# Optimization experiments

Measured on AMD Instinct MI355X. Metric: run time of the kernel, lower is better.

Reference implementation:

```python
import jax, jax.numpy as jnp
import numpy as np

N, Q, E, D = 100000, 128, 500000, 32
D4 = 4 * D
RATIO_UPDATE = 0.2
NEG_SLOPE = 0.01  # LeakyReLU default


def setup_inputs() -> dict:
    key = jax.random.key(0)
    ks = jax.random.split(key, 16)
    return {
        "visited_node_score": jax.random.uniform(ks[0], (N,), jnp.float32),
        "node_repr": jax.random.normal(ks[1], (N, D), jnp.float32),
        "eg0": jnp.sort(jax.random.randint(ks[2], (E,), 0, Q)),
        "src0": jax.random.randint(ks[3], (E,), 0, N),
        "dst0": jax.random.randint(ks[4], (E,), 0, N),
        "rel0": jax.random.normal(ks[5], (E, D), jnp.float32),
        "eg1": jnp.sort(jax.random.randint(ks[6], (E,), 0, Q)),
        "src1": jax.random.randint(ks[7], (E,), 0, N),
        "dst1": jax.random.randint(ks[8], (E,), 0, N),
        "rel1": jax.random.normal(ks[9], (E, D), jnp.float32),
        "query_src_emb": jax.random.normal(ks[10], (Q, D), jnp.float32),
        "query_rel_emb": jax.random.normal(ks[11], (Q, D), jnp.float32),
        "Wq": jax.random.normal(ks[12], (D4, D4), jnp.float32) * np.sqrt(2.0 / D4).astype(np.float32),
        "Wk": jax.random.normal(ks[13], (D4, D4), jnp.float32) * np.sqrt(2.0 / D4).astype(np.float32),
        "Wlin": jax.random.normal(ks[14], (D, D), jnp.float32) * np.sqrt(2.0 / (2 * D)).astype(np.float32),
        "blin": jnp.zeros((D,), jnp.float32),
        "max_edges": 500,
    }


def segment_softmax(logits, seg, num_segments):
    # softmax within groups of identical seg id (source node index)
    m = jax.ops.segment_max(logits, seg, num_segments=num_segments)
    ex = jnp.exp(logits - m[seg])
    s = jax.ops.segment_sum(ex, seg, num_segments=num_segments)
    return ex / s[seg]


def segment_topk_mask(values, seg, k):
    # keep mask for per-segment top-k (seg must be sorted); stable -> first occurrence on ties
    n = values.shape[0]
    order = jnp.lexsort((-values, seg))  # primary: seg, secondary: descending value
    seg_sorted = seg[order]
    idx = jnp.arange(n)
    is_start = jnp.concatenate([jnp.array([True]), seg_sorted[1:] != seg_sorted[:-1]])
    seg_start = jax.lax.cummax(jnp.where(is_start, idx, 0))
    rank_sorted = idx - seg_start  # rank within segment, 0 = largest
    rank = jnp.zeros((n,), jnp.int32).at[order].set(rank_sorted.astype(jnp.int32))
    return rank < k


def reference(visited_node_score, node_repr, eg0, src0, dst0, rel0,
              eg1, src1, dst1, rel1, query_src_emb, query_rel_emb,
              Wq, Wk, Wlin, blin, max_edges):
    def att_logits(repr_, src, dst, eg, rel):
        q = query_src_emb[eg]
        r = query_rel_emb[eg]
        left = jnp.concatenate([repr_[src], rel, q, r], axis=-1)   # [E, 4D]
        right = jnp.concatenate([repr_[dst], rel, q, r], axis=-1)  # [E, 4D]
        return jnp.sum((left @ Wq.T) * (right @ Wk.T), axis=-1)    # [E]

    num_nodes = node_repr.shape[0]

    # ---- last layer: attention + segmented top-k pruning ----
    logits1 = att_logits(node_repr, src1, dst1, eg1, rel1)
    w1 = segment_softmax(logits1, src1, num_nodes)           # softmax over out-edges of each src node
    src_score = visited_node_score[src1]
    target_score = w1 * src_score
    keep = segment_topk_mask(target_score, eg1, max_edges)   # top-k per eg_idx
    w1p = jnp.where(keep, w1, 0.0)

    # node score aggregation == 'sum': score[n] = sum_{kept e: dst=n} w * src_score
    updated_node_score = jax.ops.segment_sum(w1p * src_score, dst1, num_segments=num_nodes)

    # representation update along pruned edges (linear_act=False)
    agg = jax.ops.segment_sum(w1p[:, None] * node_repr[src1], dst1, num_segments=num_nodes)
    repr_ = (1.0 - RATIO_UPDATE) * agg + RATIO_UPDATE * node_repr

    # ---- earlier layer(s), no pruning ----
    logits0 = att_logits(repr_, src0, dst0, eg0, rel0)
    w0 = segment_softmax(logits0, src0, num_nodes)
    agg0 = jax.ops.segment_sum(w0[:, None] * repr_[src0], dst0, num_segments=num_nodes)
    repr_ = (1.0 - RATIO_UPDATE) * agg0 + RATIO_UPDATE * repr_

    # bypass_forward: LeakyReLU(Linear(repr))
    h = repr_ @ Wlin.T + blin
    updated_repr = jnp.where(h >= 0, h, NEG_SLOPE * h)
    return updated_node_score, updated_repr
```

## Files before the change

### kernel.cpp

```cpp
#include <hip/hip_runtime.h>
#include <math.h>

#define DD 32
#define DD4 128
#define TPB 256
#define LDSCAP 6144
#define CANDCAP 2048

__device__ __forceinline__ unsigned long long dsort_key(double x) {
  unsigned long long b = (unsigned long long)__double_as_longlong(x);
  return (b & 0x8000000000000000ull) ? ~b : (b | 0x8000000000000000ull);
}
__device__ __forceinline__ double dunsort_key(unsigned long long k) {
  unsigned long long b = (k & 0x8000000000000000ull) ? (k ^ 0x8000000000000000ull) : ~k;
  return __longlong_as_double((long long)b);
}
__device__ __forceinline__ unsigned int fsort_key(float x) {
  unsigned int b = __float_as_uint(x);
  return (b & 0x80000000u) ? ~b : (b | 0x80000000u);
}
__device__ __forceinline__ float funsort_key(unsigned int k) {
  unsigned int b = (k & 0x80000000u) ? (k ^ 0x80000000u) : ~k;
  return __uint_as_float(b);
}

__device__ __forceinline__ int block_iscan256(int x, int* wsum) {
  const int lane = threadIdx.x & 63, w = threadIdx.x >> 6;
#pragma unroll
  for (int o = 1; o < 64; o <<= 1) {
    int y = __shfl_up(x, o, 64);
    if (lane >= o) x += y;
  }
  if (lane == 63) wsum[w] = x;
  __syncthreads();
  int add = 0;
#pragma unroll
  for (int i = 0; i < 4; ++i) add += (i < w) ? wsum[i] : 0;
  __syncthreads();
  return x + add;
}

__global__ __launch_bounds__(TPB) void k_precompute_M(
    const float* __restrict__ Wq, const float* __restrict__ Wk,
    double* __restrict__ M64) {
  int t = blockIdx.x * blockDim.x + threadIdx.x;
  int i = t >> 7, j = t & 127;
  double acc = 0.0;
  for (int k = 0; k < DD4; ++k)
    acc += (double)Wq[k * DD4 + i] * (double)Wk[k * DD4 + j];
  M64[i * DD4 + j] = acc;
}

__global__ __launch_bounds__(TPB) void k_sym22(
    const double* __restrict__ M64, double* __restrict__ S64) {
  int i = blockIdx.x * blockDim.x + threadIdx.x;
  int r = i >> 5, c = i & 31;
  double g  = M64[(32 + r) * DD4 + 32 + c];
  double gt = M64[(32 + c) * DD4 + 32 + r];
  S64[i] = (c > r) ? (g + gt) : ((c == r) ? g : 0.0);
}

__global__ __launch_bounds__(64) void k_per_query(
    const double* __restrict__ M64,
    const float* __restrict__ qemb, const float* __restrict__ remb,
    double* __restrict__ p64, double* __restrict__ pD64, double* __restrict__ c64,
    float* __restrict__ p32, float* __restrict__ pD32, float* __restrict__ c32) {
  int q = blockIdx.x;
  int l = threadIdx.x;
  __shared__ double qr[64];
  qr[l] = (l < DD) ? (double)qemb[q * DD + l] : (double)remb[q * DD + (l - DD)];
  __syncthreads();
  double a = 0.0;
  for (int j = 0; j < 64; ++j) a += M64[l * DD4 + 64 + j] * qr[j];
  double ct = 0.0;
  for (int j = 0; j < 64; ++j) ct += M64[(64 + j) * DD4 + l] * qr[j];
  if (l >= DD) a += ct;
  p64[q * 64 + l] = a;
  p32[q * 64 + l] = (float)a;
  if (l < DD) {
    pD64[q * DD + l] = ct;
    pD32[q * DD + l] = (float)ct;
  }
  double a3 = 0.0;
  for (int j = 0; j < 64; ++j) a3 += M64[(64 + l) * DD4 + 64 + j] * qr[j];
  a3 *= qr[l];
  for (int o = 32; o; o >>= 1) a3 += __shfl_xor(a3, o);
  if (l == 0) { c64[q] = a3; c32[q] = (float)a3; }
}

template <typename T, bool MIX>
__global__ __launch_bounds__(TPB) void k_node_pre(
    const double* __restrict__ M64, const float* __restrict__ reprIn,
    const float* __restrict__ aggIn, float* __restrict__ reprOut,
    float* __restrict__ t, float* __restrict__ u, float* __restrict__ v, int N_) {
  __shared__ T GT[3 * 32 * 32];
  for (int i = threadIdx.x; i < 1024; i += TPB) {
    int j = i >> 5, c = i & 31;
    GT[i]        = (T)M64[c * DD4 + j];
    GT[1024 + i] = (T)M64[j * DD4 + 32 + c];
    GT[2048 + i] = (T)M64[(32 + c) * DD4 + j];
  }
  __syncthreads();
  const int base = blockIdx.x * 32;
  const int sub = threadIdx.x >> 5;
  const int c = threadIdx.x & 31;
#pragma unroll
  for (int m = 0; m < 4; ++m) {
    const int n = base + m * 8 + sub;
    if (n >= N_) continue;
    float h = reprIn[(size_t)n * DD + c];
    if constexpr (MIX) {
      float a = aggIn[(size_t)n * DD + c];
      h = 0.8f * a + 0.2f * h;
      reprOut[(size_t)n * DD + c] = h;
    }
    T ta = (T)0, ua = (T)0, va = (T)0;
#pragma unroll
    for (int j = 0; j < 32; ++j) {
      T hj = (T)__shfl(h, j, 32);
      ta += GT[j * 32 + c] * hj;
      ua += GT[1024 + j * 32 + c] * hj;
      va += GT[2048 + j * 32 + c] * hj;
    }
    t[(size_t)n * DD + c] = (float)ta;
    u[(size_t)n * DD + c] = (float)ua;
    v[(size_t)n * DD + c] = (float)va;
  }
}

template <typename T>
__global__ __launch_bounds__(TPB) void k_quad(
    const double* __restrict__ S64,
    const float* __restrict__ rel, const int* __restrict__ eg,
    const T* __restrict__ pq, const T* __restrict__ cq,
    T* __restrict__ quad, int E) {
  __shared__ T Ss[32 * 32];
  for (int i = threadIdx.x; i < 1024; i += TPB) Ss[i] = (T)S64[i];
  __syncthreads();
  const int e = blockIdx.x * TPB + threadIdx.x;
  if (e >= E) return;
  const int q = eg[e];
  T rl[32];
  {
    const float4* r4 = (const float4*)rel + (size_t)e * 8;
#pragma unroll
    for (int j = 0; j < 8; ++j) {
      float4 x = r4[j];
      rl[4 * j] = (T)x.x; rl[4 * j + 1] = (T)x.y;
      rl[4 * j + 2] = (T)x.z; rl[4 * j + 3] = (T)x.w;
    }
  }
  const T* prow = pq + (size_t)q * 64 + 32;
  T lin0 = (T)0, lin1 = (T)0;
#pragma unroll
  for (int i = 0; i < 32; i += 2) {
    lin0 += prow[i] * rl[i];
    lin1 += prow[i + 1] * rl[i + 1];
  }
  T a0 = cq[q] + lin0, a1 = lin1, a2 = (T)0, a3 = (T)0;
#pragma unroll
  for (int i = 0; i < 32; ++i) {
    T r0 = Ss[i * 32 + i] * rl[i];
    T r1 = (T)0;
#pragma unroll
    for (int j = i + 1; j < 32; ++j) {
      if ((j - i) & 1) r1 += Ss[i * 32 + j] * rl[j];
      else             r0 += Ss[i * 32 + j] * rl[j];
    }
    T rr = (r0 + r1) * rl[i];
    if ((i & 3) == 0) a0 += rr;
    else if ((i & 3) == 1) a1 += rr;
    else if ((i & 3) == 2) a2 += rr;
    else a3 += rr;
  }
  quad[e] = (a0 + a1) + (a2 + a3);
}

template <typename T>
__global__ __launch_bounds__(TPB) void k_edge_dots(
    const float* __restrict__ repr, const float* __restrict__ rel,
    const int* __restrict__ src, const int* __restrict__ dst, const int* __restrict__ eg,
    const float* __restrict__ tvec, const float* __restrict__ uvec, const float* __restrict__ vvec,
    const T* __restrict__ pq, const T* __restrict__ pDq, const T* __restrict__ quad,
    T* __restrict__ logits, void* __restrict__ mkey, int E) {
  const long long t = (long long)blockIdx.x * TPB + threadIdx.x;
  const int e = (int)(t >> 3), part = (int)(t & 7);
  if (e >= E) return;
  const int s = src[e], d = dst[e], q = eg[e];
  const float4 hs = ((const float4*)repr)[(size_t)s * 8 + part];
  const float4 td = ((const float4*)tvec)[(size_t)d * 8 + part];
  const float4 hd = ((const float4*)repr)[(size_t)d * 8 + part];
  const float4 rl = ((const float4*)rel)[(size_t)e * 8 + part];
  const float4 us = ((const float4*)uvec)[(size_t)s * 8 + part];
  const float4 vd = ((const float4*)vvec)[(size_t)d * 8 + part];
  const T* p  = pq  + (size_t)q * 64 + part * 4;
  const T* pD = pDq + (size_t)q * DD + part * 4;
  T a = (T)hs.x * ((T)td.x + p[0]) + (T)hs.y * ((T)td.y + p[1]) +
        (T)hs.z * ((T)td.z + p[2]) + (T)hs.w * ((T)td.w + p[3]);
  a += (T)hd.x * pD[0] + (T)hd.y * pD[1] + (T)hd.z * pD[2] + (T)hd.w * pD[3];
  a += (T)rl.x * (T)(us.x + vd.x) + (T)rl.y * (T)(us.y + vd.y) +
       (T)rl.z * (T)(us.z + vd.z) + (T)rl.w * (T)(us.w + vd.w);
  a += __shfl_xor(a, 1);
  a += __shfl_xor(a, 2);
  a += __shfl_xor(a, 4);
  if (part == 0) {
    a += quad[e];
    logits[e] = a;
    if constexpr (sizeof(T) == 8) {
      atomicMax((unsigned long long*)mkey + s, dsort_key((double)a));
    } else {
      atomicMax((unsigned int*)mkey + s, fsort_key((float)a));
    }
  }
}

__global__ __launch_bounds__(TPB) void k_expsum64(
    double* __restrict__ io, const unsigned long long* __restrict__ mkey,
    const int* __restrict__ src, double* __restrict__ ssum, int E) {
  int e = blockIdx.x * blockDim.x + threadIdx.x;
  if (e >= E) return;
  int s = src[e];
  double ex = exp(io[e] - dunsort_key(mkey[s]));
  io[e] = ex;
  atomicAdd(&ssum[s], ex);
}
__global__ __launch_bounds__(TPB) void k_expsum32h(
    float* __restrict__ io, const unsigned int* __restrict__ mkey,
    const int* __restrict__ src, const int* __restrict__ dst,
    float* __restrict__ ssum, int* __restrict__ cnt, int E) {
  int e = blockIdx.x * blockDim.x + threadIdx.x;
  if (e >= E) return;
  int s = src[e];
  float ex = expf(io[e] - funsort_key(mkey[s]));
  io[e] = ex;
  atomicAdd(&ssum[s], ex);
  atomicAdd(&cnt[dst[e]], 1);
}

__global__ __launch_bounds__(TPB) void k_weights_target(
    const double* __restrict__ ex, const double* __restrict__ ssum,
    const int* __restrict__ src, const float* __restrict__ score,
    const int* __restrict__ eg, int* __restrict__ qoff,
    float* __restrict__ w1f, unsigned int* __restrict__ tkey, int E, int Q) {
  int e = blockIdx.x * blockDim.x + threadIdx.x;
  if (e >= E) return;
  int s = src[e];
  double w = ex[e] / ssum[s];
  float wf = (float)w;
  w1f[e] = wf;
  float tgt = wf * score[s];
  tkey[e] = fsort_key(tgt);
  int cur = eg[e];
  int prev = (e == 0) ? -1 : eg[e - 1];
  for (int v = prev + 1; v <= cur; ++v) qoff[v] = e;
  if (e == E - 1) {
    for (int v = cur + 1; v <= Q; ++v) qoff[v] = E;
  }
}

__global__ __launch_bounds__(TPB) void k_topk(
    const unsigned int* __restrict__ tkey, const float* __restrict__ w1f,
    const int* __restrict__ qoff, const int* __restrict__ maxe,
    float* __restrict__ w1p, int E) {
  __shared__ unsigned int keys[LDSCAP];
  __shared__ int hist[256];
  __shared__ unsigned short cand[CANDCAP];
  __shared__ int wsum[4];
  __shared__ int sh_cnt;
  __shared__ unsigned int sh_prefix;
  __shared__ int sh_need;
  const int q = blockIdx.x;
  const int s = qoff[q], e2 = qoff[q + 1];
  const int n = e2 - s;
  const int K = maxe[0];
  if (n <= K) {
    for (int i = s + threadIdx.x; i < e2; i += TPB) w1p[i] = w1f[i];
    return;
  }
  const bool useLds = (n <= LDSCAP);
  if (useLds) {
    for (int i = threadIdx.x; i < n; i += TPB) keys[i] = tkey[s + i];
  }
  hist[threadIdx.x] = 0;
  __syncthreads();
  for (int i = threadIdx.x; i < n; i += TPB) {
    unsigned int k = useLds ? keys[i] : tkey[s + i];
    atomicAdd(&hist[k >> 24], 1);
  }
  __syncthreads();
  int need = K;
  {
    int h = hist[255 - threadIdx.x];
    int incl = block_iscan256(h, wsum);
    int excl = incl - h;
    if (incl >= need && excl < need) {
      sh_prefix = (unsigned int)(255 - threadIdx.x) << 24;
      sh_need = need - excl;
    }
  }
  __syncthreads();
  unsigned int prefix = sh_prefix;
  need = sh_need;
  const int cnt0 = hist[prefix >> 24];
  const bool compact = useLds && (cnt0 <= CANDCAP);
  if (threadIdx.x == 0) sh_cnt = 0;
  __syncthreads();
  if (compact) {
    const unsigned int d0 = prefix >> 24;
    for (int i = threadIdx.x; i < n; i += TPB) {
      if ((keys[i] >> 24) == d0) {
        int p = atomicAdd(&sh_cnt, 1);
        cand[p] = (unsigned short)i;
      }
    }
  }
  __syncthreads();
  const int ncand = compact ? sh_cnt : 0;
  for (int pass = 1; pass < 4; ++pass) {
    const int shift = 24 - 8 * pass;
    const unsigned int himask = 0xFFFFFFFFu << (shift + 8);
    hist[threadIdx.x] = 0;
    __syncthreads();
    if (compact) {
      for (int ci = threadIdx.x; ci < ncand; ci += TPB) {
        unsigned int k = keys[cand[ci]];
        if ((k & himask) == prefix) atomicAdd(&hist[(k >> shift) & 255], 1);
      }
    } else {
      for (int i = threadIdx.x; i < n; i += TPB) {
        unsigned int k = useLds ? keys[i] : tkey[s + i];
        if ((k & himask) == prefix) atomicAdd(&hist[(k >> shift) & 255], 1);
      }
    }
    __syncthreads();
    int h = hist[255 - threadIdx.x];
    int incl = block_iscan256(h, wsum);
    int excl = incl - h;
    if (incl >= need && excl < need) {
      sh_prefix = prefix | ((unsigned int)(255 - threadIdx.x) << shift);
      sh_need = need - excl;
    }
    __syncthreads();
    prefix = sh_prefix;
    need = sh_need;
    __syncthreads();
  }
  const unsigned int kth = prefix;
  const int r = need;
  const int C = (n + TPB - 1) / TPB;
  const int b0 = min(threadIdx.x * C, n);
  const int b1 = min(b0 + C, n);
  int myt = 0;
  for (int i = b0; i < b1; ++i) {
    unsigned int k = useLds ? keys[i] : tkey[s + i];
    myt += (k == kth) ? 1 : 0;
  }
  int tincl = block_iscan256(myt, wsum);
  int tiepre = tincl - myt;
  for (int i = b0; i < b1; ++i) {
    unsigned int k = useLds ? keys[i] : tkey[s + i];
    float v = 0.f;
    if (k > kth) {
      v = w1f[s + i];
    } else if (k == kth) {
      if (tiepre < r) v = w1f[s + i];
      ++tiepre;
    }
    w1p[s + i] = v;
  }
}

__global__ __launch_bounds__(TPB) void k_apply1(
    const float* __restrict__ w1p, const int* __restrict__ src, const int* __restrict__ dst,
    const float* __restrict__ repr0, const float* __restrict__ score,
    float* __restrict__ agg, float* __restrict__ score_out, int E) {
  int t = blockIdx.x * blockDim.x + threadIdx.x;
  int e = t >> 3, part = t & 7;
  if (e >= E) return;
  float w = w1p[e];
  if (w == 0.f) return;
  int sv = src[e], dv = dst[e];
  const float4 rv = ((const float4*)repr0)[sv * 8 + part];
  float* ap = agg + (size_t)dv * DD + part * 4;
  atomicAdd(ap + 0, w * rv.x);
  atomicAdd(ap + 1, w * rv.y);
  atomicAdd(ap + 2, w * rv.z);
  atomicAdd(ap + 3, w * rv.w);
  if (part == 0) atomicAdd(score_out + dv, w * score[sv]);
}

#define SCHUNK 1024
__global__ __launch_bounds__(TPB) void k_scan1(
    const int* __restrict__ cnt, int* __restrict__ off, int* __restrict__ bsum, int N_) {
  __shared__ int sd[TPB];
  const int b = blockIdx.x, t = threadIdx.x;
  const int base = b * SCHUNK + t * 4;
  int v[4];
  int s4 = 0;
#pragma unroll
  for (int k = 0; k < 4; ++k) {
    v[k] = (base + k < N_) ? cnt[base + k] : 0;
    s4 += v[k];
  }
  sd[t] = s4;
  __syncthreads();
  for (int o = 1; o < TPB; o <<= 1) {
    int x = (t >= o) ? sd[t - o] : 0;
    __syncthreads();
    sd[t] += x;
    __syncthreads();
  }
  int excl = sd[t] - s4;
  if (t == TPB - 1) bsum[b] = sd[t];
  int run = excl;
#pragma unroll
  for (int k = 0; k < 4; ++k) {
    if (base + k < N_) { off[base + k] = run; run += v[k]; }
  }
}

__global__ __launch_bounds__(TPB) void k_scan2(
    int* __restrict__ bsum, int* __restrict__ off, int nblk, int N_, int E) {
  __shared__ int wsum[4];
  if (nblk <= TPB) {
    int t = threadIdx.x;
    int x = (t < nblk) ? bsum[t] : 0;
    int orig = x;
    const int lane = t & 63, w = t >> 6;
#pragma unroll
    for (int o = 1; o < 64; o <<= 1) {
      int y = __shfl_up(x, o, 64);
      if (lane >= o) x += y;
    }
    if (lane == 63) wsum[w] = x;
    __syncthreads();
    int add = 0;
#pragma unroll
    for (int i = 0; i < 4; ++i) add += (i < w) ? wsum[i] : 0;
    x += add;
    if (t < nblk) bsum[t] = x - orig;
    if (t == 0) off[N_] = E;
  } else {
    if (threadIdx.x != 0) return;
    int run = 0;
    for (int i = 0; i < nblk; ++i) { int tmp = bsum[i]; bsum[i] = run; run += tmp; }
    off[N_] = E;
  }
}

__global__ __launch_bounds__(TPB) void k_scan3(
    int* __restrict__ off, const int* __restrict__ bsum, int* __restrict__ cursor, int N_) {
  int i = blockIdx.x * blockDim.x + threadIdx.x;
  if (i >= N_) return;
  int v = off[i] + bsum[i >> 10];
  off[i] = v;
  cursor[i] = v;
}

__global__ __launch_bounds__(TPB) void k_scatter0(
    const float* __restrict__ ex, const float* __restrict__ ssum,
    const int* __restrict__ src, const int* __restrict__ dst,
    int* __restrict__ cursor, float2* __restrict__ pk, int E) {
  int e = blockIdx.x * blockDim.x + threadIdx.x;
  if (e >= E) return;
  int s = src[e];
  float w = ex[e] / ssum[s];
  int pos = atomicAdd(&cursor[dst[e]], 1);
  pk[pos] = make_float2(w, __int_as_float(s));
}

__global__ __launch_bounds__(TPB) void k_gather_final(
    const float2* __restrict__ pk, const int* __restrict__ off,
    const float* __restrict__ repr1,
    const float* __restrict__ Wlin, const float* __restrict__ blin,
    float* __restrict__ out_repr, int N_) {
  __shared__ float WsT[DD * DD];
  __shared__ float bs[DD];
  for (int i = threadIdx.x; i < DD * DD; i += TPB) {
    int r = i >> 5, c = i & 31;
    WsT[c * DD + r] = Wlin[i];
  }
  if (threadIdx.x < DD) bs[threadIdx.x] = blin[threadIdx.x];
  __syncthreads();
  const int n = blockIdx.x * 8 + (threadIdx.x >> 5);
  const int c = threadIdx.x & 31;
  if (n >= N_) return;
  float acc = 0.f;
  const int j1 = off[n + 1];
  for (int j = off[n]; j < j1; ++j) {
    float2 p = pk[j];
    int s = __float_as_int(p.y);
    acc += p.x * repr1[(size_t)s * DD + c];
  }
  float mix = 0.8f * acc + 0.2f * repr1[(size_t)n * DD + c];
  float o = bs[c];
#pragma unroll 8
  for (int j = 0; j < DD; ++j) {
    float mj = __shfl(mix, j, 32);
    o += WsT[j * DD + c] * mj;
  }
  out_repr[(size_t)n * DD + c] = (o >= 0.f) ? o : 0.01f * o;
}

extern "C" void kernel_launch(void* const* d_in, const int* in_sizes, int n_in,
                              void* d_out, int out_size, void* d_ws, size_t ws_size,
                              hipStream_t stream) {
  (void)n_in; (void)out_size; (void)ws_size;
  const float* score = (const float*)d_in[0];
  const float* nrepr = (const float*)d_in[1];
  const int*   eg0   = (const int*)d_in[2];
  const int*   src0  = (const int*)d_in[3];
  const int*   dst0  = (const int*)d_in[4];
  const float* rel0  = (const float*)d_in[5];
  const int*   eg1   = (const int*)d_in[6];
  const int*   src1  = (const int*)d_in[7];
  const int*   dst1  = (const int*)d_in[8];
  const float* rel1  = (const float*)d_in[9];
  const float* qemb  = (const float*)d_in[10];
  const float* remb  = (const float*)d_in[11];
  const float* Wq    = (const float*)d_in[12];
  const float* Wk    = (const float*)d_in[13];
  const float* Wlin  = (const float*)d_in[14];
  const float* blin  = (const float*)d_in[15];
  const int*   maxe  = (const int*)d_in[16];

  const int N_ = in_sizes[0];
  const int E_ = in_sizes[2];
  const int Q_ = in_sizes[10] / DD;

  char* wsc = (char*)d_ws;
  size_t off = 0;
  auto alloc = [&](size_t bytes) -> void* {
    void* p = wsc + off;
    off += (bytes + 255) & ~(size_t)255;
    return p;
  };
  double* M64  = (double*)alloc((size_t)DD4 * DD4 * 8);
  double* S64  = (double*)alloc((size_t)DD * DD * 8);
  double* p64  = (double*)alloc((size_t)Q_ * 64 * 8);
  double* pD64 = (double*)alloc((size_t)Q_ * DD * 8);
  double* c64  = (double*)alloc((size_t)Q_ * 8);
  float*  p32  = (float*)alloc((size_t)Q_ * 64 * 4);
  float*  pD32 = (float*)alloc((size_t)Q_ * DD * 4);
  float*  c32  = (float*)alloc((size_t)Q_ * 4);
  int*    qoff = (int*)alloc((size_t)(Q_ + 2) * 4);
  double* lg1  = (double*)alloc((size_t)E_ * 8);
  double* qv64 = (double*)alloc((size_t)E_ * 8);
  float*  w1f  = (float*)alloc((size_t)E_ * 4);
  unsigned int* tkey = (unsigned int*)alloc((size_t)E_ * 4);
  float*  w1p  = (float*)alloc((size_t)E_ * 4);
  float*  lg0  = (float*)alloc((size_t)E_ * 4);
  float*  repr1 = (float*)alloc((size_t)N_ * DD * 4);
  float*  tvec = (float*)alloc((size_t)N_ * DD * 4);
  float*  uvec = (float*)alloc((size_t)N_ * DD * 4);
  float*  vvec = (float*)alloc((size_t)N_ * DD * 4);
  size_t zstart = off;
  unsigned long long* mkey1 = (unsigned long long*)alloc((size_t)N_ * 8);
  double* s1   = (double*)alloc((size_t)N_ * 8);
  float*  agg  = (float*)alloc((size_t)N_ * DD * 4);
  unsigned int* mkey0 = (unsigned int*)alloc((size_t)N_ * 4);
  float*  s0   = (float*)alloc((size_t)N_ * 4);
  size_t zlen = off - zstart;

  float* qv32 = (float*)qv64;

  int* cnt    = (int*)tvec;
  int* offcsr = (int*)tvec + N_;
  int* cursor = (int*)tvec + 2 * (size_t)N_ + 64;
  int* bsum   = (int*)tvec + 3 * (size_t)N_ + 128;
  float2* pk  = (float2*)uvec;

  float* out_score = (float*)d_out;
  float* out_repr  = out_score + N_;

  hipMemsetAsync(wsc + zstart, 0, zlen, stream);
  hipMemsetAsync(d_out, 0, (size_t)N_ * 4, stream);

  k_precompute_M<<<(DD4 * DD4) / TPB, TPB, 0, stream>>>(Wq, Wk, M64);
  k_sym22<<<4, TPB, 0, stream>>>(M64, S64);
  k_per_query<<<Q_, 64, 0, stream>>>(M64, qemb, remb, p64, pD64, c64, p32, pD32, c32);

  const int ngrid = (N_ + TPB - 1) / TPB;
  const int n32grid = (N_ + 31) / 32;
  const int egrid = (E_ + TPB - 1) / TPB;
  const int dgrid = (int)(((size_t)E_ * 8 + TPB - 1) / TPB);

  k_node_pre<double, false><<<n32grid, TPB, 0, stream>>>(M64, nrepr, nullptr, nullptr,
                                                         tvec, uvec, vvec, N_);
  k_quad<double><<<egrid, TPB, 0, stream>>>(S64, rel1, eg1, p64, c64, qv64, E_);
  k_edge_dots<double><<<dgrid, TPB, 0, stream>>>(nrepr, rel1, src1, dst1, eg1,
                                                 tvec, uvec, vvec, p64, pD64, qv64,
                                                 lg1, (void*)mkey1, E_);
  k_expsum64<<<egrid, TPB, 0, stream>>>(lg1, mkey1, src1, s1, E_);
  k_weights_target<<<egrid, TPB, 0, stream>>>(lg1, s1, src1, score, eg1, qoff,
                                              w1f, tkey, E_, Q_);
  k_topk<<<Q_, TPB, 0, stream>>>(tkey, w1f, qoff, maxe, w1p, E_);

  k_apply1<<<dgrid, TPB, 0, stream>>>(w1p, src1, dst1, nrepr, score, agg, out_score, E_);

  k_node_pre<float, true><<<n32grid, TPB, 0, stream>>>(M64, nrepr, agg, repr1,
                                                       tvec, uvec, vvec, N_);
  k_quad<float><<<egrid, TPB, 0, stream>>>(S64, rel0, eg0, p32, c32, qv32, E_);
  k_edge_dots<float><<<dgrid, TPB, 0, stream>>>(repr1, rel0, src0, dst0, eg0,
                                                tvec, uvec, vvec, p32, pD32, qv32,
                                                lg0, (void*)mkey0, E_);

  hipMemsetAsync(cnt, 0, (size_t)N_ * 4, stream);
  k_expsum32h<<<egrid, TPB, 0, stream>>>(lg0, mkey0, src0, dst0, s0, cnt, E_);
  const int nblk = (N_ + SCHUNK - 1) / SCHUNK;
  k_scan1<<<nblk, TPB, 0, stream>>>(cnt, offcsr, bsum, N_);
  k_scan2<<<1, TPB, 0, stream>>>(bsum, offcsr, nblk, N_, E_);
  k_scan3<<<ngrid, TPB, 0, stream>>>(offcsr, bsum, cursor, N_);
  k_scatter0<<<egrid, TPB, 0, stream>>>(lg0, s0, src0, dst0, cursor, pk, E_);
  k_gather_final<<<(N_ + 7) / 8, TPB, 0, stream>>>(pk, offcsr, repr1, Wlin, blin, out_repr, N_);
}
```

Measured before the change: 688.5 us.

## Restructure node projection to one node per thread with uniform matrix reads

k_node_pre now assigns one node per thread. Each thread holds its 32-element representation in registers and reads the projection matrices directly from global memory with thread-uniform addresses, replacing the LDS-staged matrix and per-element warp shuffles. Outputs are transposed through LDS so global stores stay coalesced as float4. k_quad also drops its LDS staging of the symmetric matrix and reads it uniformly from global, and float32 copies of M and S are precomputed so the float passes skip per-block double-to-float conversion. This adds register pressure (32 accumulator inputs plus 8 partial sums) and several extra block barriers per kernel.

```diff
diff --git a/kernel.cpp b/kernel.cpp
--- a/kernel.cpp
+++ b/kernel.cpp
@@ -42,22 +42,25 @@
 
 __global__ __launch_bounds__(TPB) void k_precompute_M(
     const float* __restrict__ Wq, const float* __restrict__ Wk,
-    double* __restrict__ M64) {
+    double* __restrict__ M64, float* __restrict__ M32) {
   int t = blockIdx.x * blockDim.x + threadIdx.x;
   int i = t >> 7, j = t & 127;
   double acc = 0.0;
   for (int k = 0; k < DD4; ++k)
     acc += (double)Wq[k * DD4 + i] * (double)Wk[k * DD4 + j];
   M64[i * DD4 + j] = acc;
+  M32[i * DD4 + j] = (float)acc;
 }
 
 __global__ __launch_bounds__(TPB) void k_sym22(
-    const double* __restrict__ M64, double* __restrict__ S64) {
+    const double* __restrict__ M64, double* __restrict__ S64, float* __restrict__ S32) {
   int i = blockIdx.x * blockDim.x + threadIdx.x;
   int r = i >> 5, c = i & 31;
   double g  = M64[(32 + r) * DD4 + 32 + c];
   double gt = M64[(32 + c) * DD4 + 32 + r];
-  S64[i] = (c > r) ? (g + gt) : ((c == r) ? g : 0.0);
+  double s = (c > r) ? (g + gt) : ((c == r) ? g : 0.0);
+  S64[i] = s;
+  S32[i] = (float)s;
 }
 
 __global__ __launch_bounds__(64) void k_per_query(
@@ -88,55 +91,86 @@
   if (l == 0) { c64[q] = a3; c32[q] = (float)a3; }
 }
 
+#define G_T(c) Mmat[(c) * DD4 + j]
+#define G_U(c) Mmat[j * DD4 + 32 + (c)]
+#define G_V(c) Mmat[(32 + (c)) * DD4 + j]
+
+#define NP_TILE(GEXPR)                                                          \
+  for (int tt = 0; tt < 4; ++tt) {                                              \
+    T a0=(T)0,a1=(T)0,a2=(T)0,a3=(T)0,a4=(T)0,a5=(T)0,a6=(T)0,a7=(T)0;          \
+    const int c0 = tt * 8;                                                      \
+    _Pragma("unroll")                                                           \
+    for (int j = 0; j < 32; ++j) {                                              \
+      const T hj = hh[j];                                                       \
+      a0 += (GEXPR(c0 + 0)) * hj; a1 += (GEXPR(c0 + 1)) * hj;                   \
+      a2 += (GEXPR(c0 + 2)) * hj; a3 += (GEXPR(c0 + 3)) * hj;                   \
+      a4 += (GEXPR(c0 + 4)) * hj; a5 += (GEXPR(c0 + 5)) * hj;                   \
+      a6 += (GEXPR(c0 + 6)) * hj; a7 += (GEXPR(c0 + 7)) * hj;                   \
+    }                                                                           \
+    xq[tid * 9 + tt * 2]     = make_float4((float)a0,(float)a1,(float)a2,(float)a3); \
+    xq[tid * 9 + tt * 2 + 1] = make_float4((float)a4,(float)a5,(float)a6,(float)a7); \
+  }
+
+#define NP_STORE(dst)                                                           \
+  __syncthreads();                                                              \
+  {                                                                             \
+    float4* go = (float4*)(dst) + (size_t)nbase * 8;                            \
+    _Pragma("unroll")                                                           \
+    for (int k = 0; k < 8; ++k) {                                               \
+      int f = k * TPB + tid;                                                    \
+      if ((f >> 3) < nlim) go[f] = xq[(f >> 3) * 9 + (f & 7)];                  \
+    }                                                                           \
+  }                                                                             \
+  __syncthreads();
+
 template <typename T, bool MIX>
 __global__ __launch_bounds__(TPB) void k_node_pre(
-    const double* __restrict__ M64, const float* __restrict__ reprIn,
+    const T* __restrict__ Mmat, const float* __restrict__ reprIn,
     const float* __restrict__ aggIn, float* __restrict__ reprOut,
     float* __restrict__ t, float* __restrict__ u, float* __restrict__ v, int N_) {
-  __shared__ T GT[3 * 32 * 32];
-  for (int i = threadIdx.x; i < 1024; i += TPB) {
-    int j = i >> 5, c = i & 31;
-    GT[i]        = (T)M64[c * DD4 + j];
-    GT[1024 + i] = (T)M64[j * DD4 + 32 + c];
-    GT[2048 + i] = (T)M64[(32 + c) * DD4 + j];
-  }
-  __syncthreads();
-  const int base = blockIdx.x * 32;
-  const int sub = threadIdx.x >> 5;
-  const int c = threadIdx.x & 31;
-#pragma unroll
-  for (int m = 0; m < 4; ++m) {
-    const int n = base + m * 8 + sub;
-    if (n >= N_) continue;
-    float h = reprIn[(size_t)n * DD + c];
-    if constexpr (MIX) {
-      float a = aggIn[(size_t)n * DD + c];
-      h = 0.8f * a + 0.2f * h;
-      reprOut[(size_t)n * DD + c] = h;
-    }
-    T ta = (T)0, ua = (T)0, va = (T)0;
-#pragma unroll
-    for (int j = 0; j < 32; ++j) {
-      T hj = (T)__shfl(h, j, 32);
-      ta += GT[j * 32 + c] * hj;
-      ua += GT[1024 + j * 32 + c] * hj;
-      va += GT[2048 + j * 32 + c] * hj;
-    }
-    t[(size_t)n * DD + c] = (float)ta;
-    u[(size_t)n * DD + c] = (float)ua;
-    v[(size_t)n * DD + c] = (float)va;
-  }
+  __shared__ float xp[TPB * 36];
+  float4* xq = (float4*)xp;
+  const int tid = threadIdx.x;
+  const int nbase = blockIdx.x * TPB;
+  const int n = nbase + tid;
+  const int nlim = min(TPB, N_ - nbase);
+  const bool valid = tid < nlim;
+  T hh[32];
+  if (valid) {
+    const float4* h4 = (const float4*)reprIn + (size_t)n * 8;
+#pragma unroll
+    for (int jq = 0; jq < 8; ++jq) {
+      float4 x = h4[jq];
+      if constexpr (MIX) {
+        const float4 a = ((const float4*)aggIn)[(size_t)n * 8 + jq];
+        x = make_float4(0.8f * a.x + 0.2f * x.x, 0.8f * a.y + 0.2f * x.y,
+                        0.8f * a.z + 0.2f * x.z, 0.8f * a.w + 0.2f * x.w);
+        xq[tid * 9 + jq] = x;
+      }
+      hh[4 * jq]     = (T)x.x; hh[4 * jq + 1] = (T)x.y;
+      hh[4 * jq + 2] = (T)x.z; hh[4 * jq + 3] = (T)x.w;
+    }
+  } else {
+#pragma unroll
+    for (int j = 0; j < 32; ++j) hh[j] = (T)0;
+  }
+  if constexpr (MIX) {
+    NP_STORE(reprOut)
+  }
+  NP_TILE(G_T)
+  NP_STORE(t)
+  NP_TILE(G_U)
+  NP_STORE(u)
+  NP_TILE(G_V)
+  NP_STORE(v)
 }
 
 template <typename T>
 __global__ __launch_bounds__(TPB) void k_quad(
-    const double* __restrict__ S64,
+    const T* __restrict__ Smat,
     const float* __restrict__ rel, const int* __restrict__ eg,
     const T* __restrict__ pq, const T* __restrict__ cq,
     T* __restrict__ quad, int E) {
-  __shared__ T Ss[32 * 32];
-  for (int i = threadIdx.x; i < 1024; i += TPB) Ss[i] = (T)S64[i];
-  __syncthreads();
   const int e = blockIdx.x * TPB + threadIdx.x;
   if (e >= E) return;
   const int q = eg[e];
@@ -160,12 +194,12 @@
   T a0 = cq[q] + lin0, a1 = lin1, a2 = (T)0, a3 = (T)0;
 #pragma unroll
   for (int i = 0; i < 32; ++i) {
-    T r0 = Ss[i * 32 + i] * rl[i];
+    T r0 = Smat[i * 32 + i] * rl[i];
     T r1 = (T)0;
 #pragma unroll
     for (int j = i + 1; j < 32; ++j) {
-      if ((j - i) & 1) r1 += Ss[i * 32 + j] * rl[j];
-      else             r0 += Ss[i * 32 + j] * rl[j];
+      if ((j - i) & 1) r1 += Smat[i * 32 + j] * rl[j];
+      else             r0 += Smat[i * 32 + j] * rl[j];
     }
     T rr = (r0 + r1) * rl[i];
     if ((i & 3) == 0) a0 += rr;
@@ -536,7 +570,9 @@
     return p;
   };
   double* M64  = (double*)alloc((size_t)DD4 * DD4 * 8);
+  float*  M32  = (float*)alloc((size_t)DD4 * DD4 * 4);
   double* S64  = (double*)alloc((size_t)DD * DD * 8);
+  float*  S32  = (float*)alloc((size_t)DD * DD * 4);
   double* p64  = (double*)alloc((size_t)Q_ * 64 * 8);
   double* pD64 = (double*)alloc((size_t)Q_ * DD * 8);
   double* c64  = (double*)alloc((size_t)Q_ * 8);
@@ -576,17 +612,16 @@
   hipMemsetAsync(wsc + zstart, 0, zlen, stream);
   hipMemsetAsync(d_out, 0, (size_t)N_ * 4, stream);
 
-  k_precompute_M<<<(DD4 * DD4) / TPB, TPB, 0, stream>>>(Wq, Wk, M64);
-  k_sym22<<<4, TPB, 0, stream>>>(M64, S64);
+  k_precompute_M<<<(DD4 * DD4) / TPB, TPB, 0, stream>>>(Wq, Wk, M64, M32);
+  k_sym22<<<4, TPB, 0, stream>>>(M64, S64, S32);
   k_per_query<<<Q_, 64, 0, stream>>>(M64, qemb, remb, p64, pD64, c64, p32, pD32, c32);
 
   const int ngrid = (N_ + TPB - 1) / TPB;
-  const int n32grid = (N_ + 31) / 32;
   const int egrid = (E_ + TPB - 1) / TPB;
   const int dgrid = (int)(((size_t)E_ * 8 + TPB - 1) / TPB);
 
-  k_node_pre<double, false><<<n32grid, TPB, 0, stream>>>(M64, nrepr, nullptr, nullptr,
-                                                         tvec, uvec, vvec, N_);
+  k_node_pre<double, false><<<ngrid, TPB, 0, stream>>>(M64, nrepr, nullptr, nullptr,
+                                                       tvec, uvec, vvec, N_);
   k_quad<double><<<egrid, TPB, 0, stream>>>(S64, rel1, eg1, p64, c64, qv64, E_);
   k_edge_dots<double><<<dgrid, TPB, 0, stream>>>(nrepr, rel1, src1, dst1, eg1,
                                                  tvec, uvec, vvec, p64, pD64, qv64,
@@ -598,9 +633,9 @@
 
   k_apply1<<<dgrid, TPB, 0, stream>>>(w1p, src1, dst1, nrepr, score, agg, out_score, E_);
 
-  k_node_pre<float, true><<<n32grid, TPB, 0, stream>>>(M64, nrepr, agg, repr1,
-                                                       tvec, uvec, vvec, N_);
-  k_quad<float><<<egrid, TPB, 0, stream>>>(S64, rel0, eg0, p32, c32, qv32, E_);
+  k_node_pre<float, true><<<ngrid, TPB, 0, stream>>>(M32, nrepr, agg, repr1,
+                                                     tvec, uvec, vvec, N_);
+  k_quad<float><<<egrid, TPB, 0, stream>>>(S32, rel0, eg0, p32, c32, qv32, E_);
   k_edge_dots<float><<<dgrid, TPB, 0, stream>>>(repr1, rel0, src0, dst0, eg0,
                                                 tvec, uvec, vvec, p32, pD32, qv32,
                                                 lg0, (void*)mkey0, E_);
```

After: 637.9 us. 1.08x faster.
